# Optimization experiments

Hardware: AMD Instinct MI355X
Metric: run time of the kernel (lower is better)

Reference implementation:

```python
import jax, jax.numpy as jnp
import numpy as np

H = 128      # hidden_size
B = 8192     # number of sessions
L = 50       # items per session (constant here; code supports ragged)
T = B * L    # total tokens


def setup_inputs() -> dict:
    key = jax.random.key(0)
    ks = jax.random.split(key, 10)
    s = 1.0 / np.sqrt(H)
    u = lambda k, shape: jax.random.uniform(k, shape, jnp.float32, -s, s)
    return {
        "intra_item_emb": jax.random.normal(ks[0], (T, H), jnp.float32),
        "inter_item_emb": jax.random.normal(ks[1], (T, H), jnp.float32),
        "W1": u(ks[2], (H, H)), "b1": u(ks[3], (H,)),
        "W2": u(ks[4], (H, H)), "b2": u(ks[5], (H,)),
        "q_w": u(ks[6], (1, H)), "q_b": u(ks[7], (1,)),
        "W3": u(ks[8], (H, 2 * H)), "b3": u(ks[9], (H,)),
        "seq_len": jnp.full((B,), L, dtype=jnp.int32),
    }


def reference(intra_item_emb, inter_item_emb, W1, b1, W2, b2, q_w, q_b, W3, b3, seq_len):
    # max_fusing: elementwise max of the two embedding streams  [T, H]
    hidden = jnp.maximum(intra_item_emb, inter_item_emb)
    nB = seq_len.shape[0]
    nT = hidden.shape[0]
    # segment id per token and index of last token of each session
    seg_ids = jnp.repeat(jnp.arange(nB), seq_len, total_repeat_length=nT)  # [T]
    last_idx = jnp.cumsum(seq_len) - 1                                      # [B]
    v_n = hidden[last_idx]                 # [B, H] last node of each session
    v_n_rep = v_n[seg_ids]                 # [T, H] broadcast last node to tokens
    # attention weight per token: q(sigmoid(W1 v_n + W2 h))  [T, 1]
    alpha = jax.nn.sigmoid(v_n_rep @ W1.T + b1 + hidden @ W2.T + b2) @ q_w.T + q_b
    # segment-sum pooling of alpha-weighted tokens  [B, H]
    s_g = jax.ops.segment_sum(alpha * hidden, seg_ids, num_segments=nB)
    # final session representation  [B, H]
    h_s = jnp.concatenate([v_n, s_g], axis=1) @ W3.T + b3
    return h_s
```

## Files before the change

### kernel.cpp

```cpp
#include <hip/hip_runtime.h>
#include <hip/hip_bf16.h>

#define HDIM 128
#define RS 136

typedef __attribute__((ext_vector_type(8))) short short8;
typedef __attribute__((ext_vector_type(4))) float floatv4;

static __device__ __forceinline__ unsigned short f2bf(float f) {
  union { float f; unsigned u; } x; x.f = f;
  unsigned r = x.u + 0x7fffu + ((x.u >> 16) & 1u);
  return (unsigned short)(r >> 16);
}
static __device__ __forceinline__ float blo(unsigned u) { return __uint_as_float(u << 16); }
static __device__ __forceinline__ float bhi(unsigned u) { return __uint_as_float(u & 0xffff0000u); }

static __device__ __forceinline__ void glds16(const void* g, const void* l) {
  __builtin_amdgcn_global_load_lds(
      (const __attribute__((address_space(1))) unsigned int*)(unsigned long long)g,
      (__attribute__((address_space(3))) unsigned int*)(unsigned long long)l, 16, 0, 0);
}
static __device__ __forceinline__ void glds4(const void* g, const void* l) {
  __builtin_amdgcn_global_load_lds(
      (const __attribute__((address_space(1))) unsigned int*)(unsigned long long)g,
      (__attribute__((address_space(3))) unsigned int*)(unsigned long long)l, 4, 0, 0);
}

static __device__ __forceinline__ void sync_lds() {
  asm volatile("s_waitcnt lgkmcnt(0)" ::: "memory");
  __builtin_amdgcn_s_barrier();
  asm volatile("" ::: "memory");
}
static __device__ __forceinline__ void sync_all() {
  asm volatile("s_waitcnt vmcnt(0) lgkmcnt(0)" ::: "memory");
  __builtin_amdgcn_s_barrier();
  asm volatile("" ::: "memory");
}

static __device__ __forceinline__ void dma_session(
    const float* __restrict__ intra, const float* __restrict__ inter,
    int start, int n, float* rawA, float* rawB, int wid, int lane) {
  const char* ga = (const char*)(intra + (size_t)start * HDIM);
  const char* gb = (const char*)(inter + (size_t)start * HDIM);
  char* la = (char*)rawA;
  char* lb = (char*)rawB;
  int nfull = n >> 1;
  for (int i = wid; i < nfull; i += 4) {
    int off = i << 10;
    glds16(ga + off + (lane << 4), la + off);
    glds16(gb + off + (lane << 4), lb + off);
  }
  if ((n & 1) && wid == 0) {
    int off = (n - 1) << 9;
    glds4(ga + off + (lane << 2), la + off);
    glds4(ga + off + 256 + (lane << 2), la + off + 256);
    glds4(gb + off + (lane << 2), lb + off);
    glds4(gb + off + 256 + (lane << 2), lb + off + 256);
  }
}

__global__ void prep_kernel(const int* __restrict__ seq, int* __restrict__ offs, int B,
                            const float* __restrict__ W1, const float* __restrict__ W2,
                            const float* __restrict__ W3,
                            unsigned short* __restrict__ w1b, unsigned short* __restrict__ w2b,
                            unsigned short* __restrict__ w3b) {
  if (blockIdx.x == 0) {
    __shared__ int part[256];
    int tid = threadIdx.x;
    int chunk = (B + 255) >> 8;
    int beg = tid * chunk, end = min(beg + chunk, B);
    int s = 0;
    for (int i = beg; i < end; ++i) s += seq[i];
    part[tid] = s;
    __syncthreads();
    for (int d = 1; d < 256; d <<= 1) {
      int v = (tid >= d) ? part[tid - d] : 0;
      __syncthreads();
      part[tid] += v;
      __syncthreads();
    }
    int run = (tid == 0) ? 0 : part[tid - 1];
    for (int i = beg; i < end; ++i) { offs[i] = run; run += seq[i]; }
  } else {
    int i = (blockIdx.x - 1) * 256 + threadIdx.x;
    if (i < 16384) { w1b[i] = f2bf(W1[i]); w2b[i] = f2bf(W2[i]); }
    if (i < 32768) { w3b[i] = f2bf(W3[i]); }
  }
}

__global__ __launch_bounds__(256, 1) void session_kernel(
    const float* __restrict__ intra, const float* __restrict__ inter,
    const unsigned short* __restrict__ w1b, const float* __restrict__ b1,
    const unsigned short* __restrict__ w2b, const float* __restrict__ b2,
    const float* __restrict__ qw, const float* __restrict__ qb,
    const unsigned short* __restrict__ w3b, const float* __restrict__ b3,
    const int* __restrict__ seq, const int* __restrict__ offs,
    float* __restrict__ out, int B) {
  __shared__ float rawA[2][64 * HDIM];
  __shared__ float rawB[2][64 * HDIM];
  __shared__ unsigned short hbf[64 * RS];
  __shared__ unsigned short vnb[HDIM];
  __shared__ unsigned short sgb[HDIM];
  __shared__ float alphaAcc[64];
  __shared__ float sgpart[4][HDIM];

  const int tid = threadIdx.x;
  const int lane = tid & 63, wid = tid >> 6;
  const int quad = lane >> 4, lcol = lane & 15;
  const int nbase = wid << 5;
  const int n0 = nbase + lcol, n1 = n0 + 16;
  const int G = gridDim.x;

  const float qb0 = qb[0];
  const float bb0 = b1[n0] + b2[n0], bb1 = b1[n1] + b2[n1];
  const float q0 = qw[n0], q1 = qw[n1];
  const float b30 = b3[n0], b31 = b3[n1];

  short8 w1f[2][4], w2f[2][4], w3f[2][8];
  #pragma unroll
  for (int kt = 0; kt < 4; ++kt) {
    w1f[0][kt] = *(const short8*)(w1b + n0 * HDIM + (kt << 5) + (quad << 3));
    w1f[1][kt] = *(const short8*)(w1b + n1 * HDIM + (kt << 5) + (quad << 3));
    w2f[0][kt] = *(const short8*)(w2b + n0 * HDIM + (kt << 5) + (quad << 3));
    w2f[1][kt] = *(const short8*)(w2b + n1 * HDIM + (kt << 5) + (quad << 3));
  }
  #pragma unroll
  for (int kt = 0; kt < 8; ++kt) {
    w3f[0][kt] = *(const short8*)(w3b + n0 * 256 + (kt << 5) + (quad << 3));
    w3f[1][kt] = *(const short8*)(w3b + n1 * 256 + (kt << 5) + (quad << 3));
  }

  int n_cur;
  {
    int s0 = blockIdx.x;
    n_cur = seq[s0]; if (n_cur > 64) n_cur = 64;
    dma_session(intra, inter, offs[s0], n_cur, rawA[0], rawB[0], wid, lane);
  }
  int cur = 0;

  for (int s = blockIdx.x; s < B; s += G) {
    const int sn = s + G;
    int n_nxt = 0, st_nxt = 0;
    if (sn < B) {
      n_nxt = seq[sn]; if (n_nxt > 64) n_nxt = 64;
      st_nxt = offs[sn];
    }

    sync_all();

    if (sn < B)
      dma_session(intra, inter, st_nxt, n_nxt, rawA[cur ^ 1], rawB[cur ^ 1], wid, lane);
    asm volatile("" ::: "memory");

    {
      const float4* a4 = (const float4*)rawA[cur];
      const float4* c4 = (const float4*)rawB[cur];
      const int lastrow = (n_cur > 0) ? (n_cur - 1) : 0;
      #pragma unroll
      for (int it = 0; it < 8; ++it) {
        int idx = (it << 8) + tid;
        int t = idx >> 5, j4 = idx & 31;
        float4 r; r.x = 0.f; r.y = 0.f; r.z = 0.f; r.w = 0.f;
        if (t < n_cur) {
          float4 a = a4[idx], c = c4[idx];
          r.x = fmaxf(a.x, c.x); r.y = fmaxf(a.y, c.y);
          r.z = fmaxf(a.z, c.z); r.w = fmaxf(a.w, c.w);
        }
        union { __hip_bfloat162 b; unsigned u; } p01, p23;
        p01.b = __float22bfloat162_rn(make_float2(r.x, r.y));
        p23.b = __float22bfloat162_rn(make_float2(r.z, r.w));
        uint2 st; st.x = p01.u; st.y = p23.u;
        *(uint2*)&hbf[t * RS + (j4 << 2)] = st;
        if (t == lastrow) *(uint2*)&vnb[j4 << 2] = st;
      }
      if (tid < 64) alphaAcc[tid] = qb0;
    }
    sync_lds();

    float c0, c1;
    {
      floatv4 p0 = {0.f, 0.f, 0.f, 0.f}, p1 = {0.f, 0.f, 0.f, 0.f};
      #pragma unroll
      for (int kt = 0; kt < 4; ++kt) {
        short8 af = *(const short8*)&vnb[(kt << 5) + (quad << 3)];
        p0 = __builtin_amdgcn_mfma_f32_16x16x32_bf16(af, w1f[0][kt], p0, 0, 0, 0);
        p1 = __builtin_amdgcn_mfma_f32_16x16x32_bf16(af, w1f[1][kt], p1, 0, 0, 0);
      }
      c0 = p0[0] + bb0;
      c1 = p1[0] + bb1;
    }

    #pragma unroll
    for (int mt = 0; mt < 4; ++mt) {
      floatv4 a0 = {c0, c0, c0, c0}, a1 = {c1, c1, c1, c1};
      const unsigned short* arow = &hbf[((mt << 4) + lcol) * RS + (quad << 3)];
      #pragma unroll
      for (int kt = 0; kt < 4; ++kt) {
        short8 af = *(const short8*)(arow + (kt << 5));
        a0 = __builtin_amdgcn_mfma_f32_16x16x32_bf16(af, w2f[0][kt], a0, 0, 0, 0);
        a1 = __builtin_amdgcn_mfma_f32_16x16x32_bf16(af, w2f[1][kt], a1, 0, 0, 0);
      }
      #pragma unroll
      for (int r = 0; r < 4; ++r) {
        float v = q0 * __builtin_amdgcn_rcpf(1.f + __expf(-a0[r]))
                + q1 * __builtin_amdgcn_rcpf(1.f + __expf(-a1[r]));
        v += __shfl_xor(v, 1, 64);
        v += __shfl_xor(v, 2, 64);
        v += __shfl_xor(v, 4, 64);
        v += __shfl_xor(v, 8, 64);
        if (lcol == 0) atomicAdd(&alphaAcc[(mt << 4) + (quad << 2) + r], v);
      }
    }
    sync_lds();

    {
      int jg = tid & 15, ts = tid >> 4;
      float ac[8];
      #pragma unroll
      for (int e = 0; e < 8; ++e) ac[e] = 0.f;
      #pragma unroll
      for (int tt = 0; tt < 4; ++tt) {
        int t = (tt << 4) + ts;
        float al = alphaAcc[t];
        uint4 u = *(const uint4*)&hbf[t * RS + (jg << 3)];
        ac[0] += al * blo(u.x); ac[1] += al * bhi(u.x);
        ac[2] += al * blo(u.y); ac[3] += al * bhi(u.y);
        ac[4] += al * blo(u.z); ac[5] += al * bhi(u.z);
        ac[6] += al * blo(u.w); ac[7] += al * bhi(u.w);
      }
      #pragma unroll
      for (int e = 0; e < 8; ++e) {
        ac[e] += __shfl_xor(ac[e], 16, 64);
        ac[e] += __shfl_xor(ac[e], 32, 64);
      }
      if (quad == 0) {
        float4 s0v; s0v.x = ac[0]; s0v.y = ac[1]; s0v.z = ac[2]; s0v.w = ac[3];
        float4 s1v; s1v.x = ac[4]; s1v.y = ac[5]; s1v.z = ac[6]; s1v.w = ac[7];
        *(float4*)&sgpart[wid][(jg << 3)] = s0v;
        *(float4*)&sgpart[wid][(jg << 3) + 4] = s1v;
      }
    }
    sync_lds();
    if (tid < HDIM) {
      float sv = sgpart[0][tid] + sgpart[1][tid] + sgpart[2][tid] + sgpart[3][tid];
      sgb[tid] = f2bf(sv);
    }
    sync_lds();

    {
      floatv4 o0 = {0.f, 0.f, 0.f, 0.f}, o1 = {0.f, 0.f, 0.f, 0.f};
      #pragma unroll
      for (int kt = 0; kt < 8; ++kt) {
        const unsigned short* src = (kt < 4) ? &vnb[kt << 5] : &sgb[(kt - 4) << 5];
        short8 af = *(const short8*)(src + (quad << 3));
        o0 = __builtin_amdgcn_mfma_f32_16x16x32_bf16(af, w3f[0][kt], o0, 0, 0, 0);
        o1 = __builtin_amdgcn_mfma_f32_16x16x32_bf16(af, w3f[1][kt], o1, 0, 0, 0);
      }
      if (quad == 0) {
        out[(size_t)s * HDIM + n0] = o0[0] + b30;
        out[(size_t)s * HDIM + n1] = o1[0] + b31;
      }
    }

    cur ^= 1;
    n_cur = n_nxt;
  }
}

extern "C" void kernel_launch(void* const* d_in, const int* in_sizes, int n_in,
                              void* d_out, int out_size, void* d_ws, size_t ws_size,
                              hipStream_t stream) {
  const float* intra = (const float*)d_in[0];
  const float* inter = (const float*)d_in[1];
  const float* W1 = (const float*)d_in[2];
  const float* b1 = (const float*)d_in[3];
  const float* W2 = (const float*)d_in[4];
  const float* b2 = (const float*)d_in[5];
  const float* qw = (const float*)d_in[6];
  const float* qb = (const float*)d_in[7];
  const float* W3 = (const float*)d_in[8];
  const float* b3 = (const float*)d_in[9];
  const int* seq = (const int*)d_in[10];
  const int B = in_sizes[10];
  float* out = (float*)d_out;

  char* ws = (char*)d_ws;
  size_t o1 = (((size_t)B * 4) + 255) & ~(size_t)255;
  int* offs = (int*)ws;
  unsigned short* w1b = (unsigned short*)(ws + o1);
  unsigned short* w2b = (unsigned short*)(ws + o1 + 32768);
  unsigned short* w3b = (unsigned short*)(ws + o1 + 65536);

  int nblk = B < 256 ? B : 256;

  hipLaunchKernelGGL(prep_kernel, dim3(129), dim3(256), 0, stream,
                     seq, offs, B, W1, W2, W3, w1b, w2b, w3b);
  hipLaunchKernelGGL(session_kernel, dim3(nblk), dim3(256), 0, stream,
                     intra, inter, w1b, b1, w2b, b2, qw, qb, w3b, b3, seq, offs, out, B);
}
```

Measured before the change: 532.6 us.

## Precompute fused bf16 hidden tensor and run session kernel at higher occupancy

```diff
diff --git a/kernel.cpp b/kernel.cpp
--- a/kernel.cpp
+++ b/kernel.cpp
@@ -35,28 +35,6 @@
   asm volatile("s_waitcnt vmcnt(0) lgkmcnt(0)" ::: "memory");
   __builtin_amdgcn_s_barrier();
   asm volatile("" ::: "memory");
-}
-
-static __device__ __forceinline__ void dma_session(
-    const float* __restrict__ intra, const float* __restrict__ inter,
-    int start, int n, float* rawA, float* rawB, int wid, int lane) {
-  const char* ga = (const char*)(intra + (size_t)start * HDIM);
-  const char* gb = (const char*)(inter + (size_t)start * HDIM);
-  char* la = (char*)rawA;
-  char* lb = (char*)rawB;
-  int nfull = n >> 1;
-  for (int i = wid; i < nfull; i += 4) {
-    int off = i << 10;
-    glds16(ga + off + (lane << 4), la + off);
-    glds16(gb + off + (lane << 4), lb + off);
-  }
-  if ((n & 1) && wid == 0) {
-    int off = (n - 1) << 9;
-    glds4(ga + off + (lane << 2), la + off);
-    glds4(ga + off + 256 + (lane << 2), la + off + 256);
-    glds4(gb + off + (lane << 2), lb + off);
-    glds4(gb + off + 256 + (lane << 2), lb + off + 256);
-  }
 }
 
 __global__ void prep_kernel(const int* __restrict__ seq, int* __restrict__ offs, int B,
@@ -88,7 +66,248 @@
   }
 }
 
-__global__ __launch_bounds__(256, 1) void session_kernel(
+__global__ __launch_bounds__(256) void fuse_kernel(
+    const float* __restrict__ intra, const float* __restrict__ inter,
+    unsigned short* __restrict__ hg, long ngroups) {
+  long stride = (long)gridDim.x * 256;
+  for (long i = (long)blockIdx.x * 256 + threadIdx.x; i < ngroups; i += stride) {
+    long t = i >> 4;
+    int g = (int)(i & 15);
+    const float4* pa = (const float4*)intra + (t << 5) + (g << 1);
+    const float4* pb = (const float4*)inter + (t << 5) + (g << 1);
+    float4 a0 = pa[0], a1 = pa[1];
+    float4 c0 = pb[0], c1 = pb[1];
+    union { __hip_bfloat162 b; unsigned u; } p0, p1, p2, p3;
+    p0.b = __float22bfloat162_rn(make_float2(fmaxf(a0.x, c0.x), fmaxf(a0.y, c0.y)));
+    p1.b = __float22bfloat162_rn(make_float2(fmaxf(a0.z, c0.z), fmaxf(a0.w, c0.w)));
+    p2.b = __float22bfloat162_rn(make_float2(fmaxf(a1.x, c1.x), fmaxf(a1.y, c1.y)));
+    p3.b = __float22bfloat162_rn(make_float2(fmaxf(a1.z, c1.z), fmaxf(a1.w, c1.w)));
+    uint4 o; o.x = p0.u; o.y = p1.u; o.z = p2.u; o.w = p3.u;
+    int gs = g ^ (int)(t & 7);
+    *(uint4*)(hg + t * HDIM + (gs << 3)) = o;
+  }
+}
+
+static __device__ __forceinline__ void dma_tile(
+    const unsigned short* __restrict__ hg, int start, int n,
+    unsigned short* dst, int wid, int lane) {
+  const char* g = (const char*)(hg + (size_t)start * HDIM);
+  char* l = (char*)dst;
+  int nf = n >> 2;
+  for (int c = wid; c < nf; c += 4) {
+    int off = c << 10;
+    glds16(g + off + (lane << 4), l + off);
+  }
+  if (wid == 0) {
+    for (int r = nf << 2; r < n; ++r) {
+      int off = r << 8;
+      glds4(g + off + (lane << 2), l + off);
+    }
+  }
+}
+
+static __device__ __forceinline__ void zero_tail(unsigned short* dst, int n, int tid) {
+  int cnt = (64 - n) << 4;
+  uint4 z; z.x = 0u; z.y = 0u; z.z = 0u; z.w = 0u;
+  for (int i = tid; i < cnt; i += 256)
+    *(uint4*)(dst + (n << 7) + (i << 3)) = z;
+}
+
+__global__ __launch_bounds__(256, 3) void session_kernel(
+    const unsigned short* __restrict__ hg,
+    const unsigned short* __restrict__ w1b, const float* __restrict__ b1,
+    const unsigned short* __restrict__ w2b, const float* __restrict__ b2,
+    const float* __restrict__ qw, const float* __restrict__ qb,
+    const unsigned short* __restrict__ w3b, const float* __restrict__ b3,
+    const int* __restrict__ seq, const int* __restrict__ offs,
+    float* __restrict__ out, int B) {
+  __shared__ __align__(16) unsigned short hb[2][64 * HDIM];
+  __shared__ __align__(16) unsigned short vnb[HDIM];
+  __shared__ __align__(16) unsigned short sgb[HDIM];
+  __shared__ float alphaAcc[64];
+  __shared__ __align__(16) float sgpart[4][HDIM];
+
+  const int tid = threadIdx.x;
+  const int lane = tid & 63, wid = tid >> 6;
+  const int quad = lane >> 4, lcol = lane & 15;
+  const int nbase = wid << 5;
+  const int n0 = nbase + lcol, n1 = n0 + 16;
+  const int G = gridDim.x;
+
+  const float qb0 = qb[0];
+  const float bb0 = b1[n0] + b2[n0], bb1 = b1[n1] + b2[n1];
+  const float q0 = qw[n0], q1 = qw[n1];
+  const float b30 = b3[n0], b31 = b3[n1];
+
+  short8 w2f[2][4], w3f[2][8];
+  #pragma unroll
+  for (int kt = 0; kt < 4; ++kt) {
+    w2f[0][kt] = *(const short8*)(w2b + n0 * HDIM + (kt << 5) + (quad << 3));
+    w2f[1][kt] = *(const short8*)(w2b + n1 * HDIM + (kt << 5) + (quad << 3));
+  }
+  #pragma unroll
+  for (int kt = 0; kt < 8; ++kt) {
+    w3f[0][kt] = *(const short8*)(w3b + n0 * 256 + (kt << 5) + (quad << 3));
+    w3f[1][kt] = *(const short8*)(w3b + n1 * 256 + (kt << 5) + (quad << 3));
+  }
+
+  int n_cur, st_cur;
+  {
+    int s0 = blockIdx.x;
+    n_cur = seq[s0]; if (n_cur > 64) n_cur = 64;
+    st_cur = offs[s0];
+    dma_tile(hg, st_cur, n_cur, hb[0], wid, lane);
+    zero_tail(hb[0], n_cur, tid);
+  }
+  int cur = 0;
+
+  for (int s = blockIdx.x; s < B; s += G) {
+    const int sn = s + G;
+    int n_nxt = 0, st_nxt = 0;
+    if (sn < B) { n_nxt = seq[sn]; if (n_nxt > 64) n_nxt = 64; st_nxt = offs[sn]; }
+
+    unsigned vnr = 0;
+    {
+      int tl = st_cur + n_cur - 1; if (tl < 0) tl = 0;
+      if (tid < 64) {
+        int gsw = (tid >> 2) ^ (tl & 7);
+        vnr = *(const unsigned*)((const char*)hg + (size_t)tl * 256 +
+                                 (gsw << 4) + ((tid & 3) << 2));
+      }
+    }
+
+    sync_all();
+
+    if (tid < 64) { *(unsigned*)&vnb[tid << 1] = vnr; alphaAcc[tid] = qb0; }
+    sync_lds();
+
+    float c0, c1;
+    {
+      floatv4 p0 = {0.f, 0.f, 0.f, 0.f}, p1 = {0.f, 0.f, 0.f, 0.f};
+      #pragma unroll
+      for (int kt = 0; kt < 4; ++kt) {
+        short8 af = *(const short8*)&vnb[(kt << 5) + (quad << 3)];
+        short8 bf0 = *(const short8*)(w1b + n0 * HDIM + (kt << 5) + (quad << 3));
+        short8 bf1 = *(const short8*)(w1b + n1 * HDIM + (kt << 5) + (quad << 3));
+        p0 = __builtin_amdgcn_mfma_f32_16x16x32_bf16(af, bf0, p0, 0, 0, 0);
+        p1 = __builtin_amdgcn_mfma_f32_16x16x32_bf16(af, bf1, p1, 0, 0, 0);
+      }
+      c0 = p0[0] + bb0;
+      c1 = p1[0] + bb1;
+    }
+
+    if (sn < B) {
+      dma_tile(hg, st_nxt, n_nxt, hb[cur ^ 1], wid, lane);
+      zero_tail(hb[cur ^ 1], n_nxt, tid);
+    }
+    asm volatile("" ::: "memory");
+
+    const unsigned short* hc = hb[cur];
+    const int st7 = st_cur & 7;
+    const int p5 = (st7 + lcol) & 7;
+    #pragma unroll
+    for (int mt = 0; mt < 4; ++mt) {
+      floatv4 a0 = {c0, c0, c0, c0}, a1 = {c1, c1, c1, c1};
+      const unsigned short* rbase = hc + ((mt << 4) + lcol) * HDIM;
+      #pragma unroll
+      for (int kt = 0; kt < 4; ++kt) {
+        int gidx = ((kt << 2) | quad) ^ p5;
+        short8 af = *(const short8*)(rbase + (gidx << 3));
+        a0 = __builtin_amdgcn_mfma_f32_16x16x32_bf16(af, w2f[0][kt], a0, 0, 0, 0);
+        a1 = __builtin_amdgcn_mfma_f32_16x16x32_bf16(af, w2f[1][kt], a1, 0, 0, 0);
+      }
+      #pragma unroll
+      for (int r = 0; r < 4; ++r) {
+        float v = q0 * __builtin_amdgcn_rcpf(1.f + __expf(-a0[r]))
+                + q1 * __builtin_amdgcn_rcpf(1.f + __expf(-a1[r]));
+        v += __shfl_xor(v, 1, 64);
+        v += __shfl_xor(v, 2, 64);
+        v += __shfl_xor(v, 4, 64);
+        v += __shfl_xor(v, 8, 64);
+        if (lcol == 0) atomicAdd(&alphaAcc[(mt << 4) + (quad << 2) + r], v);
+      }
+    }
+    sync_lds();
+
+    {
+      int jg = tid & 15, ts = tid >> 4;
+      const int p6 = (st7 + ts) & 7;
+      float ac[8];
+      #pragma unroll
+      for (int e = 0; e < 8; ++e) ac[e] = 0.f;
+      #pragma unroll
+      for (int tt = 0; tt < 4; ++tt) {
+        int t = (tt << 4) + ts;
+        float al = alphaAcc[t];
+        uint4 u = *(const uint4*)(hc + (t << 7) + ((jg ^ p6) << 3));
+        ac[0] += al * blo(u.x); ac[1] += al * bhi(u.x);
+        ac[2] += al * blo(u.y); ac[3] += al * bhi(u.y);
+        ac[4] += al * blo(u.z); ac[5] += al * bhi(u.z);
+        ac[6] += al * blo(u.w); ac[7] += al * bhi(u.w);
+      }
+      #pragma unroll
+      for (int e = 0; e < 8; ++e) {
+        ac[e] += __shfl_xor(ac[e], 16, 64);
+        ac[e] += __shfl_xor(ac[e], 32, 64);
+      }
+      if (quad == 0) {
+        float4 s0v; s0v.x = ac[0]; s0v.y = ac[1]; s0v.z = ac[2]; s0v.w = ac[3];
+        float4 s1v; s1v.x = ac[4]; s1v.y = ac[5]; s1v.z = ac[6]; s1v.w = ac[7];
+        *(float4*)&sgpart[wid][(jg << 3)] = s0v;
+        *(float4*)&sgpart[wid][(jg << 3) + 4] = s1v;
+      }
+    }
+    sync_lds();
+    if (tid < HDIM) {
+      float sv = sgpart[0][tid] + sgpart[1][tid] + sgpart[2][tid] + sgpart[3][tid];
+      sgb[tid] = f2bf(sv);
+    }
+    sync_lds();
+
+    {
+      floatv4 o0 = {0.f, 0.f, 0.f, 0.f}, o1 = {0.f, 0.f, 0.f, 0.f};
+      #pragma unroll
+      for (int kt = 0; kt < 8; ++kt) {
+        const unsigned short* src = (kt < 4) ? &vnb[kt << 5] : &sgb[(kt - 4) << 5];
+        short8 af = *(const short8*)(src + (quad << 3));
+        o0 = __builtin_amdgcn_mfma_f32_16x16x32_bf16(af, w3f[0][kt], o0, 0, 0, 0);
+        o1 = __builtin_amdgcn_mfma_f32_16x16x32_bf16(af, w3f[1][kt], o1, 0, 0, 0);
+      }
+      if (quad == 0) {
+        out[(size_t)s * HDIM + n0] = o0[0] + b30;
+        out[(size_t)s * HDIM + n1] = o1[0] + b31;
+      }
+    }
+
+    cur ^= 1;
+    n_cur = n_nxt;
+    st_cur = st_nxt;
+  }
+}
+
+static __device__ __forceinline__ void dma_session_fb(
+    const float* __restrict__ intra, const float* __restrict__ inter,
+    int start, int n, float* rawA, float* rawB, int wid, int lane) {
+  const char* ga = (const char*)(intra + (size_t)start * HDIM);
+  const char* gb = (const char*)(inter + (size_t)start * HDIM);
+  char* la = (char*)rawA;
+  char* lb = (char*)rawB;
+  int nfull = n >> 1;
+  for (int i = wid; i < nfull; i += 4) {
+    int off = i << 10;
+    glds16(ga + off + (lane << 4), la + off);
+    glds16(gb + off + (lane << 4), lb + off);
+  }
+  if ((n & 1) && wid == 0) {
+    int off = (n - 1) << 9;
+    glds4(ga + off + (lane << 2), la + off);
+    glds4(ga + off + 256 + (lane << 2), la + off + 256);
+    glds4(gb + off + (lane << 2), lb + off);
+    glds4(gb + off + 256 + (lane << 2), lb + off + 256);
+  }
+}
+
+__global__ __launch_bounds__(256, 1) void session_kernel_fb(
     const float* __restrict__ intra, const float* __restrict__ inter,
     const unsigned short* __restrict__ w1b, const float* __restrict__ b1,
     const unsigned short* __restrict__ w2b, const float* __restrict__ b2,
@@ -134,22 +353,18 @@
   {
     int s0 = blockIdx.x;
     n_cur = seq[s0]; if (n_cur > 64) n_cur = 64;
-    dma_session(intra, inter, offs[s0], n_cur, rawA[0], rawB[0], wid, lane);
+    dma_session_fb(intra, inter, offs[s0], n_cur, rawA[0], rawB[0], wid, lane);
   }
   int cur = 0;
 
   for (int s = blockIdx.x; s < B; s += G) {
     const int sn = s + G;
     int n_nxt = 0, st_nxt = 0;
-    if (sn < B) {
-      n_nxt = seq[sn]; if (n_nxt > 64) n_nxt = 64;
-      st_nxt = offs[sn];
-    }
+    if (sn < B) { n_nxt = seq[sn]; if (n_nxt > 64) n_nxt = 64; st_nxt = offs[sn]; }
 
     sync_all();
-
     if (sn < B)
-      dma_session(intra, inter, st_nxt, n_nxt, rawA[cur ^ 1], rawB[cur ^ 1], wid, lane);
+      dma_session_fb(intra, inter, st_nxt, n_nxt, rawA[cur ^ 1], rawB[cur ^ 1], wid, lane);
     asm volatile("" ::: "memory");
 
     {
@@ -282,6 +497,7 @@
   const float* b3 = (const float*)d_in[9];
   const int* seq = (const int*)d_in[10];
   const int B = in_sizes[10];
+  const long T = (long)in_sizes[0] / HDIM;
   float* out = (float*)d_out;
 
   char* ws = (char*)d_ws;
@@ -290,11 +506,22 @@
   unsigned short* w1b = (unsigned short*)(ws + o1);
   unsigned short* w2b = (unsigned short*)(ws + o1 + 32768);
   unsigned short* w3b = (unsigned short*)(ws + o1 + 65536);
-
-  int nblk = B < 256 ? B : 256;
+  unsigned short* hg  = (unsigned short*)(ws + o1 + 131072);
+
+  size_t needed = o1 + 131072 + (size_t)T * 256;
 
   hipLaunchKernelGGL(prep_kernel, dim3(129), dim3(256), 0, stream,
                      seq, offs, B, W1, W2, W3, w1b, w2b, w3b);
-  hipLaunchKernelGGL(session_kernel, dim3(nblk), dim3(256), 0, stream,
-                     intra, inter, w1b, b1, w2b, b2, qw, qb, w3b, b3, seq, offs, out, B);
-}
+
+  if (ws_size >= needed) {
+    hipLaunchKernelGGL(fuse_kernel, dim3(2048), dim3(256), 0, stream,
+                       intra, inter, hg, T * 16);
+    int nblk = B < 768 ? B : 768;
+    hipLaunchKernelGGL(session_kernel, dim3(nblk), dim3(256), 0, stream,
+                       hg, w1b, b1, w2b, b2, qw, qb, w3b, b3, seq, offs, out, B);
+  } else {
+    int nblk = B < 256 ? B : 256;
+    hipLaunchKernelGGL(session_kernel_fb, dim3(nblk), dim3(256), 0, stream,
+                       intra, inter, w1b, b1, w2b, b2, qw, qb, w3b, b3, seq, offs, out, B);
+  }
+}
```

Measured after the change: 555.6 us. +4.3%, slower.
